# Performance work log

Measured on AMD Instinct MI355X. Metric: run time of the kernel, lower is better.

## Reference

```python
import jax, jax.numpy as jnp
import numpy as np

HEADS = 16
KV_HEADS = 4
DIM_HEAD = 64
DIM = 1024
B, N = 2, 2048


def setup_inputs() -> dict:
    key = jax.random.key(0)
    k1, k2, k3 = jax.random.split(key, 3)
    x = jax.random.normal(k1, (B, N, DIM), dtype=jnp.float32)
    Wq = jax.random.normal(k2, (DIM, HEADS * DIM_HEAD), dtype=jnp.float32) / np.sqrt(DIM)
    Wkv = jax.random.normal(k3, (DIM, 2 * KV_HEADS * DIM_HEAD), dtype=jnp.float32) / np.sqrt(DIM)
    k_scale = jnp.ones((HEADS, 1, DIM_HEAD), dtype=jnp.float32)
    return {"x": x, "Wq": Wq, "Wkv": Wkv, "k_scale": k_scale}


def reference(x, Wq, Wkv, k_scale):
    b, n, _ = x.shape
    g = HEADS // KV_HEADS  # query heads per kv head
    scale = DIM_HEAD ** -0.5
    # fused qkv projections (no bias)
    q = (x @ Wq).reshape(b, n, HEADS, DIM_HEAD)
    kv = x @ Wkv
    k, v = jnp.split(kv, 2, axis=-1)
    k = k.reshape(b, n, KV_HEADS, DIM_HEAD).transpose(0, 2, 1, 3)  # b k n d
    v = v.reshape(b, n, KV_HEADS, DIM_HEAD).transpose(0, 2, 1, 3)  # b k n d
    # group query heads: b, kv_heads, g, n, d
    qg = q.transpose(0, 2, 1, 3).reshape(b, KV_HEADS, g, n, DIM_HEAD)
    # per-query-head k scale, applied to the group-broadcast k (qk-norm)
    ks = k_scale.reshape(KV_HEADS, g, 1, DIM_HEAD)
    kk = k[:, :, None, :, :] * ks  # b k g n d
    dots = jnp.einsum('bkgid,bkgjd->bkgij', qg, kk) * scale
    attn = jax.nn.softmax(dots, axis=-1)
    out = jnp.einsum('bkgij,bkjd->bkgid', attn, v)  # v broadcast over g
    out = out.reshape(b, HEADS, n, DIM_HEAD).transpose(0, 2, 1, 3).reshape(b, n, HEADS * DIM_HEAD)
    return out
```

## Files before the change

### kernel.cpp

```cpp
#include <hip/hip_runtime.h>
#include <stdint.h>
#include <math.h>

typedef __attribute__((ext_vector_type(8))) __bf16 bf16x8;
typedef __attribute__((ext_vector_type(4))) float f32x4;
typedef __attribute__((ext_vector_type(16))) float f32x16;

__device__ __forceinline__ uint32_t f32_to_bf16_rne(float f) {
  union { float f; uint32_t u; } v; v.f = f;
  return (v.u + 0x7FFFu + ((v.u >> 16) & 1u)) >> 16;
}

__device__ __forceinline__ uint32_t cvt_pk_bf16(float lo, float hi) {
  uint32_t r;
  asm("v_cvt_pk_bf16_f32 %0, %1, %2" : "=v"(r) : "v"(lo), "v"(hi));
  return r;
}

__device__ __forceinline__ void gld16(void* lds, const void* g) {
  __builtin_amdgcn_global_load_lds(
      (__attribute__((address_space(1))) void*)(g),
      (__attribute__((address_space(3))) void*)(lds), 16, 0, 0);
}

__device__ __forceinline__ f32x4 mfma16(bf16x8 a, bf16x8 b, f32x4 c) {
  return __builtin_amdgcn_mfma_f32_16x16x32_bf16(a, b, c, 0, 0, 0);
}
__device__ __forceinline__ f32x16 mfma32(bf16x8 a, bf16x8 b, f32x16 c) {
  return __builtin_amdgcn_mfma_f32_32x32x16_bf16(a, b, c, 0, 0, 0);
}

#define LOG2E 1.44269504088896340736f

__global__ __launch_bounds__(256) void k_convert(const float* __restrict__ x,
                                                 const float* __restrict__ wq,
                                                 const float* __restrict__ wkv,
                                                 uint16_t* __restrict__ xb,
                                                 uint16_t* __restrict__ wt) {
  __shared__ float tile[64][65];
  int blk = blockIdx.x;
  int t = threadIdx.x;
  if (blk < 2048) {
    int i = blk * 256 + t;
    const float4* xv = (const float4*)x;
    float4 a = xv[2 * i], b2 = xv[2 * i + 1];
    uint32_t w0 = f32_to_bf16_rne(a.x) | (f32_to_bf16_rne(a.y) << 16);
    uint32_t w1 = f32_to_bf16_rne(a.z) | (f32_to_bf16_rne(a.w) << 16);
    uint32_t w2 = f32_to_bf16_rne(b2.x) | (f32_to_bf16_rne(b2.y) << 16);
    uint32_t w3 = f32_to_bf16_rne(b2.z) | (f32_to_bf16_rne(b2.w) << 16);
    ((uint4*)xb)[i] = make_uint4(w0, w1, w2, w3);
  } else {
    int blk2 = blk - 2048;
    int c0 = (blk2 % 24) * 64, k0 = (blk2 / 24) * 64;
    int col = t & 63, rq = t >> 6;
#pragma unroll
    for (int rr = 0; rr < 16; rr++) {
      int r = rr * 4 + rq;
      int c = c0 + col;
      float v = (c < 1024) ? wq[(uint64_t)(k0 + r) * 1024 + c]
                           : wkv[(uint64_t)(k0 + r) * 512 + (c - 1024)];
      tile[r][col] = v;
    }
    __syncthreads();
#pragma unroll
    for (int rr = 0; rr < 16; rr++) {
      int a = rr * 4 + rq;
      wt[(uint64_t)(c0 + a) * 1024 + k0 + col] = (uint16_t)f32_to_bf16_rne(tile[col][a]);
    }
  }
}

__global__ __launch_bounds__(256, 3) void k_proj_gemm(
    const uint16_t* __restrict__ xb, const uint16_t* __restrict__ wt,
    const float* __restrict__ kscale, uint16_t* __restrict__ q_ws,
    uint16_t* __restrict__ kf_ws, uint16_t* __restrict__ vf_ws) {
  __shared__ __align__(16) uint16_t ring[4][6144];
  int t = threadIdx.x;
  int w = t >> 6, l = t & 63;
  int lq = l & 15, lg = l >> 4;
  int m0 = blockIdx.x * 128, n0 = blockIdx.y * 64;
  int wr = w >> 1, wc = w & 1;
  f32x4 acc[4][2] = {};

  auto stage = [&](int slot, int k0) {
#pragma unroll
    for (int j = 0; j < 2; j++) {
      int tt = j * 256 + t;
      int r = tt >> 2, s = tt & 3;
      int sl = s ^ ((r >> 1) & 3);
      gld16((char*)&ring[slot][0] + (j * 256 + w * 64) * 16,
            xb + (uint64_t)(m0 + r) * 1024 + k0 + sl * 8);
    }
    {
      int r = t >> 2, s = t & 3;
      int sl = s ^ ((r >> 1) & 3);
      gld16((char*)&ring[slot][4096] + (w * 64) * 16,
            wt + (uint64_t)(n0 + r) * 1024 + k0 + sl * 8);
    }
  };

  struct PFrags { bf16x8 a[4]; bf16x8 b[2]; };
  auto readFrags = [&](PFrags& F, int slot) {
    const uint16_t* As = &ring[slot][0];
    const uint16_t* Bs = &ring[slot][4096];
#pragma unroll
    for (int m = 0; m < 4; m++) {
      int r = wr * 64 + m * 16 + lq;
      int s = lg ^ ((r >> 1) & 3);
      F.a[m] = *(const bf16x8*)(As + r * 32 + s * 8);
    }
#pragma unroll
    for (int n = 0; n < 2; n++) {
      int r = wc * 32 + n * 16 + lq;
      int s = lg ^ ((r >> 1) & 3);
      F.b[n] = *(const bf16x8*)(Bs + r * 32 + s * 8);
    }
  };

  auto pbody = [&](int tt2, PFrags& C, PFrags& N) {
    int kn = (tt2 + 3) * 32;
    if (kn > 992) kn = 992;
    stage((tt2 + 3) & 3, kn);
    __builtin_amdgcn_s_setprio(1);
#pragma unroll
    for (int m = 0; m < 4; m++)
#pragma unroll
      for (int n = 0; n < 2; n++)
        acc[m][n] = mfma16(C.a[m], C.b[n], acc[m][n]);
    __builtin_amdgcn_s_setprio(0);
    int tn = tt2 + 1;
    if (tn > 31) tn = 31;
    readFrags(N, tn & 3);
    asm volatile("s_waitcnt vmcnt(3) lgkmcnt(0)" ::: "memory");
    __builtin_amdgcn_s_barrier();
  };

  stage(0, 0);
  stage(1, 32);
  stage(2, 64);
  asm volatile("s_waitcnt vmcnt(3)" ::: "memory");
  __builtin_amdgcn_s_barrier();
  PFrags FA, FB;
  readFrags(FA, 0);
  for (int sp = 0; sp < 16; ++sp) {
    pbody(2 * sp, FA, FB);
    pbody(2 * sp + 1, FB, FA);
  }

#pragma unroll
  for (int m = 0; m < 4; m++)
#pragma unroll
    for (int n = 0; n < 2; n++)
#pragma unroll
      for (int jj = 0; jj < 4; jj++) {
        int row = m0 + wr * 64 + m * 16 + 4 * lg + jj;
        int col = n0 + wc * 32 + n * 16 + lq;
        float val = acc[m][n][jj];
        int b = row >> 11, nn = row & 2047;
        if (col < 1024) {
          val *= kscale[col] * 0.125f * LOG2E;
          q_ws[((uint64_t)((b * 16 + (col >> 6)) * 2048 + nn)) * 64 + (col & 63)] =
              (uint16_t)f32_to_bf16_rne(val);
        } else if (col < 1280) {
          int kvh = (col - 1024) >> 6;
          int d = col & 63;
          int gsu = nn >> 5, lrr = nn & 31;
          int mm = d >> 4, hh = (d >> 3) & 1, el = d & 7;
          kf_ws[(uint64_t)(b * 4 + kvh) * 131072 +
                (uint64_t)((((gsu * 4 + mm) * 64) + hh * 32 + lrr) * 8 + el)] =
              (uint16_t)f32_to_bf16_rne(val);
        } else {
          int kvh = (col - 1280) >> 6;
          int d = col & 63;
          int gsu = nn >> 5, jj2 = (nn >> 4) & 1, hh = (nn >> 3) & 1, el = nn & 7;
          int dd = d >> 5, lrr = d & 31;
          vf_ws[(uint64_t)(b * 4 + kvh) * 131072 +
                (uint64_t)((((gsu * 4 + dd * 2 + jj2) * 64) + hh * 32 + lrr) * 8 + el)] =
              (uint16_t)f32_to_bf16_rne(val);
        }
      }
}

__global__ __launch_bounds__(1024, 1) void k_attn(const uint16_t* __restrict__ q_ws,
                                                  const uint16_t* __restrict__ kf_ws,
                                                  const uint16_t* __restrict__ vf_ws,
                                                  float* __restrict__ out) {
  extern __shared__ __align__(16) char smem[];

  int t = threadIdx.x, w = t >> 6, l = t & 63;
  int lr = l & 31, hi = l >> 5;
  int wq = w & 7, half = w >> 3;
  int blk = blockIdx.x;
  int c = blk & 7, j = blk >> 3;
  int b = c >> 2, kvh = c & 3;
  int h = kvh * 4 + (j >> 3), qb = j & 7;

  const uint16_t* Qb = q_ws + (uint64_t)(b * 16 + h) * 2048 * 64;
  const uint16_t* Kb = kf_ws + (uint64_t)(b * 4 + kvh) * 131072;
  const uint16_t* Vb = vf_ws + (uint64_t)(b * 4 + kvh) * 131072;
  int qrow0 = qb * 256 + wq * 32;

  bf16x8 qfrag[4];
#pragma unroll
  for (int m = 0; m < 4; m++)
    qfrag[m] = *(const bf16x8*)(Qb + (uint64_t)(qrow0 + lr) * 64 + m * 16 + hi * 8);

  f32x16 oacc[2] = {};
  float l_run = 0.f;

  const uint16_t* SbW = (((w & 7) < 4) ? Kb : Vb) + (uint64_t)half * 65536 +
                        (uint64_t)(w & 3) * 512 + l * 8;
  char* dstW = smem + w * 1024 + l * 16;

  auto stage = [&](int slot, int sul) { gld16(dstW + slot * 16384, SbW + sul * 2048); };
  auto slotbase = [&](int slot) {
    return (const uint16_t*)(smem + slot * 16384 + half * 8192);
  };

  auto finish = [&](f32x16& Tc, const uint16_t* baseC) {
    float p[16];
#pragma unroll
    for (int e = 0; e < 16; e++) p[e] = __builtin_amdgcn_exp2f(Tc[e]);
    float sm0 = ((p[0] + p[1]) + (p[2] + p[3])) + ((p[4] + p[5]) + (p[6] + p[7]));
    float sm1 = ((p[8] + p[9]) + (p[10] + p[11])) + ((p[12] + p[13]) + (p[14] + p[15]));
    l_run += sm0 + sm1;

    bf16x8 pa[2];
#pragma unroll
    for (int jj = 0; jj < 2; jj++) {
      const float* pp = p + 8 * jj;
      uint32_t X = cvt_pk_bf16(pp[0], pp[1]);
      uint32_t Z = cvt_pk_bf16(pp[2], pp[3]);
      uint32_t Y = cvt_pk_bf16(pp[4], pp[5]);
      uint32_t W2 = cvt_pk_bf16(pp[6], pp[7]);
      asm volatile("v_permlane32_swap_b32 %0, %1" : "+v"(X), "+v"(Y));
      asm volatile("v_permlane32_swap_b32 %0, %1" : "+v"(Z), "+v"(W2));
      union { uint32_t u[4]; bf16x8 v; } pu;
      pu.u[0] = X; pu.u[1] = Z; pu.u[2] = Y; pu.u[3] = W2;
      pa[jj] = pu.v;
    }

    bf16x8 vf[4];
#pragma unroll
    for (int i = 0; i < 4; i++) vf[i] = *(const bf16x8*)(baseC + (4 + i) * 512 + l * 8);
    __builtin_amdgcn_s_setprio(1);
#pragma unroll
    for (int dd = 0; dd < 2; dd++)
#pragma unroll
      for (int jj = 0; jj < 2; jj++)
        oacc[dd] = mfma32(pa[jj], vf[dd * 2 + jj], oacc[dd]);
    __builtin_amdgcn_s_setprio(0);
  };

#pragma unroll
  for (int tt = 0; tt < 6; ++tt) stage(tt, tt);
  asm volatile("s_waitcnt vmcnt(4)" ::: "memory");
  __builtin_amdgcn_s_barrier();

  for (int iv = 0; iv < 16; ++iv) {
    int a = 2 * iv;
    int s0 = a + 6, s1 = a + 7;
    if (s0 > 31) s0 = 31;
    if (s1 > 31) s1 = 31;
    stage((a + 6) & 7, s0);
    stage((a + 7) & 7, s1);

    const uint16_t* baseA = slotbase(a & 7);
    const uint16_t* baseB = slotbase((a + 1) & 7);

    bf16x8 kfA[4], kfB[4];
#pragma unroll
    for (int m = 0; m < 4; m++) kfA[m] = *(const bf16x8*)(baseA + m * 512 + l * 8);
#pragma unroll
    for (int m = 0; m < 4; m++) kfB[m] = *(const bf16x8*)(baseB + m * 512 + l * 8);

    f32x16 Ta = {}, Tb = {};
    __builtin_amdgcn_s_setprio(1);
#pragma unroll
    for (int m = 0; m < 4; m++) Ta = mfma32(kfA[m], qfrag[m], Ta);
#pragma unroll
    for (int m = 0; m < 4; m++) Tb = mfma32(kfB[m], qfrag[m], Tb);
    __builtin_amdgcn_s_setprio(0);

    finish(Ta, baseA);
    finish(Tb, baseB);

    asm volatile("s_waitcnt vmcnt(4)" ::: "memory");
    __builtin_amdgcn_s_barrier();
  }

  l_run += __shfl_xor(l_run, 32);

  asm volatile("s_waitcnt vmcnt(0)" ::: "memory");
  __syncthreads();

  float* exch = (float*)smem;
  float* exl = (float*)(smem + 65536);
  if (half == 1) {
#pragma unroll
    for (int r = 0; r < 16; r++) {
      int qr = (r & 3) + 8 * (r >> 2) + 4 * hi;
      exch[wq * 2048 + qr * 64 + lr] = oacc[0][r];
      exch[wq * 2048 + qr * 64 + 32 + lr] = oacc[1][r];
    }
    if (hi == 0) exl[wq * 32 + lr] = l_run;
  }
  __syncthreads();
  if (half == 0) {
    l_run += exl[wq * 32 + lr];
    float inv = 1.0f / l_run;
#pragma unroll
    for (int r = 0; r < 16; r++) {
      int qr = (r & 3) + 8 * (r >> 2) + 4 * hi;
      float iv = __shfl(inv, qr);
      float o0 = oacc[0][r] + exch[wq * 2048 + qr * 64 + lr];
      float o1 = oacc[1][r] + exch[wq * 2048 + qr * 64 + 32 + lr];
      float* orow = out + (uint64_t)(b * 2048 + qrow0 + qr) * 1024 + h * 64 + lr;
      orow[0] = o0 * iv;
      orow[32] = o1 * iv;
    }
  }
}

extern "C" void kernel_launch(void* const* d_in, const int* in_sizes, int n_in,
                              void* d_out, int out_size, void* d_ws, size_t ws_size,
                              hipStream_t stream) {
  const float* x = (const float*)d_in[0];
  const float* wq = (const float*)d_in[1];
  const float* wkv = (const float*)d_in[2];
  const float* kscale = (const float*)d_in[3];
  float* out = (float*)d_out;
  char* ws = (char*)d_ws;
  uint16_t* xb = (uint16_t*)(ws);
  uint16_t* wt = (uint16_t*)(ws + (8ull << 20));
  uint16_t* q_ws = (uint16_t*)(ws + (11ull << 20));
  uint16_t* kf_ws = (uint16_t*)(ws + (19ull << 20));
  uint16_t* vf_ws = (uint16_t*)(ws + (21ull << 20));

  static bool attr_set = false;
  if (!attr_set) {
    (void)hipFuncSetAttribute((const void*)k_attn,
                              hipFuncAttributeMaxDynamicSharedMemorySize, 131072);
    attr_set = true;
  }

  k_convert<<<2432, 256, 0, stream>>>(x, wq, wkv, xb, wt);
  k_proj_gemm<<<dim3(32, 24), 256, 0, stream>>>(xb, wt, kscale, q_ws, kf_ws, vf_ws);
  k_attn<<<256, 1024, 131072, stream>>>(q_ws, kf_ws, vf_ws, out);
}
```

Before: 77.45 us.

## Halve attention block to 8 waves, each wave handling two query tiles

Each wave in the attention kernel now processes 64 query rows (two 32-row MFMA tiles) rather than 32, so the block shrinks from 16 to 8 waves. Every K and V fragment read from LDS is reused across both query tiles. The staging pipeline moves from 8 slots with two key blocks per iteration to 6 slots with one key block per iteration, and each thread issues two global-to-LDS loads per stage. This cuts LDS reads and block size, but doubles accumulator registers per wave and lowers the number of waves available to hide latency.

Measured after the change: 76.78 us. About the same (-0.9%).

```diff
diff --git a/kernel.cpp b/kernel.cpp
--- a/kernel.cpp
+++ b/kernel.cpp
@@ -181,15 +181,15 @@
       }
 }
 
-__global__ __launch_bounds__(1024, 1) void k_attn(const uint16_t* __restrict__ q_ws,
-                                                  const uint16_t* __restrict__ kf_ws,
-                                                  const uint16_t* __restrict__ vf_ws,
-                                                  float* __restrict__ out) {
+__global__ __launch_bounds__(512, 1) void k_attn(const uint16_t* __restrict__ q_ws,
+                                                 const uint16_t* __restrict__ kf_ws,
+                                                 const uint16_t* __restrict__ vf_ws,
+                                                 float* __restrict__ out) {
   extern __shared__ __align__(16) char smem[];
 
   int t = threadIdx.x, w = t >> 6, l = t & 63;
   int lr = l & 31, hi = l >> 5;
-  int wq = w & 7, half = w >> 3;
+  int qg = w & 3, half = w >> 2;
   int blk = blockIdx.x;
   int c = blk & 7, j = blk >> 3;
   int b = c >> 2, kvh = c & 3;
@@ -198,32 +198,39 @@
   const uint16_t* Qb = q_ws + (uint64_t)(b * 16 + h) * 2048 * 64;
   const uint16_t* Kb = kf_ws + (uint64_t)(b * 4 + kvh) * 131072;
   const uint16_t* Vb = vf_ws + (uint64_t)(b * 4 + kvh) * 131072;
-  int qrow0 = qb * 256 + wq * 32;
-
-  bf16x8 qfrag[4];
-#pragma unroll
-  for (int m = 0; m < 4; m++)
-    qfrag[m] = *(const bf16x8*)(Qb + (uint64_t)(qrow0 + lr) * 64 + m * 16 + hi * 8);
-
-  f32x16 oacc[2] = {};
-  float l_run = 0.f;
-
-  const uint16_t* SbW = (((w & 7) < 4) ? Kb : Vb) + (uint64_t)half * 65536 +
-                        (uint64_t)(w & 3) * 512 + l * 8;
-  char* dstW = smem + w * 1024 + l * 16;
-
-  auto stage = [&](int slot, int sul) { gld16(dstW + slot * 16384, SbW + sul * 2048); };
+  int qrow0 = qb * 256 + qg * 64;
+
+  bf16x8 qfA[4], qfB[4];
+#pragma unroll
+  for (int m = 0; m < 4; m++) {
+    qfA[m] = *(const bf16x8*)(Qb + (uint64_t)(qrow0 + lr) * 64 + m * 16 + hi * 8);
+    qfB[m] = *(const bf16x8*)(Qb + (uint64_t)(qrow0 + 32 + lr) * 64 + m * 16 + hi * 8);
+  }
+
+  f32x16 oaccA[2] = {}, oaccB[2] = {};
+  float lA = 0.f, lB = 0.f;
+
+  const uint16_t* SbW = ((qg < 2) ? Kb : Vb) + (uint64_t)half * 65536 +
+                        (uint64_t)((qg & 1) * 2) * 512 + l * 8;
+  char* dstW = smem + half * 8192 + ((qg < 2) ? 0 : 4096) + (qg & 1) * 2048 + l * 16;
+
+  auto stage = [&](int slot, int sul) {
+    char* d = dstW + slot * 16384;
+    const uint16_t* s = SbW + (uint64_t)sul * 2048;
+    gld16(d, s);
+    gld16(d + 1024, s + 512);
+  };
   auto slotbase = [&](int slot) {
     return (const uint16_t*)(smem + slot * 16384 + half * 8192);
   };
 
-  auto finish = [&](f32x16& Tc, const uint16_t* baseC) {
+  auto finish = [&](f32x16& Tc, const bf16x8* vf, f32x16* oacc, float& lsum) {
     float p[16];
 #pragma unroll
     for (int e = 0; e < 16; e++) p[e] = __builtin_amdgcn_exp2f(Tc[e]);
     float sm0 = ((p[0] + p[1]) + (p[2] + p[3])) + ((p[4] + p[5]) + (p[6] + p[7]));
     float sm1 = ((p[8] + p[9]) + (p[10] + p[11])) + ((p[12] + p[13]) + (p[14] + p[15]));
-    l_run += sm0 + sm1;
+    lsum += sm0 + sm1;
 
     bf16x8 pa[2];
 #pragma unroll
@@ -240,9 +247,6 @@
       pa[jj] = pu.v;
     }
 
-    bf16x8 vf[4];
-#pragma unroll
-    for (int i = 0; i < 4; i++) vf[i] = *(const bf16x8*)(baseC + (4 + i) * 512 + l * 8);
     __builtin_amdgcn_s_setprio(1);
 #pragma unroll
     for (int dd = 0; dd < 2; dd++)
@@ -253,43 +257,41 @@
   };
 
 #pragma unroll
-  for (int tt = 0; tt < 6; ++tt) stage(tt, tt);
-  asm volatile("s_waitcnt vmcnt(4)" ::: "memory");
+  for (int tt = 0; tt < 4; ++tt) stage(tt, tt);
+  asm volatile("s_waitcnt vmcnt(6)" ::: "memory");
   __builtin_amdgcn_s_barrier();
 
-  for (int iv = 0; iv < 16; ++iv) {
-    int a = 2 * iv;
-    int s0 = a + 6, s1 = a + 7;
-    if (s0 > 31) s0 = 31;
-    if (s1 > 31) s1 = 31;
-    stage((a + 6) & 7, s0);
-    stage((a + 7) & 7, s1);
-
-    const uint16_t* baseA = slotbase(a & 7);
-    const uint16_t* baseB = slotbase((a + 1) & 7);
-
-    bf16x8 kfA[4], kfB[4];
-#pragma unroll
-    for (int m = 0; m < 4; m++) kfA[m] = *(const bf16x8*)(baseA + m * 512 + l * 8);
-#pragma unroll
-    for (int m = 0; m < 4; m++) kfB[m] = *(const bf16x8*)(baseB + m * 512 + l * 8);
+  for (int su = 0; su < 32; ++su) {
+    int sn = su + 4;
+    if (sn > 31) sn = 31;
+    stage((su + 4) % 6, sn);
+
+    const uint16_t* base = slotbase(su % 6);
+    bf16x8 kf[4];
+#pragma unroll
+    for (int m = 0; m < 4; m++) kf[m] = *(const bf16x8*)(base + m * 512 + l * 8);
 
     f32x16 Ta = {}, Tb = {};
     __builtin_amdgcn_s_setprio(1);
 #pragma unroll
-    for (int m = 0; m < 4; m++) Ta = mfma32(kfA[m], qfrag[m], Ta);
-#pragma unroll
-    for (int m = 0; m < 4; m++) Tb = mfma32(kfB[m], qfrag[m], Tb);
+    for (int m = 0; m < 4; m++) Ta = mfma32(kf[m], qfA[m], Ta);
+#pragma unroll
+    for (int m = 0; m < 4; m++) Tb = mfma32(kf[m], qfB[m], Tb);
     __builtin_amdgcn_s_setprio(0);
 
-    finish(Ta, baseA);
-    finish(Tb, baseB);
-
-    asm volatile("s_waitcnt vmcnt(4)" ::: "memory");
+    bf16x8 vf[4];
+#pragma unroll
+    for (int i = 0; i < 4; i++) vf[i] = *(const bf16x8*)(base + (4 + i) * 512 + l * 8);
+
+    finish(Ta, vf, oaccA, lA);
+    finish(Tb, vf, oaccB, lB);
+
+    asm volatile("s_waitcnt vmcnt(6)" ::: "memory");
     __builtin_amdgcn_s_barrier();
   }
 
-  l_run += __shfl_xor(l_run, 32);
+  lA += __shfl_xor(lA, 32);
+  lB += __shfl_xor(lB, 32);
 
   asm volatile("s_waitcnt vmcnt(0)" ::: "memory");
   __syncthreads();
@@ -298,26 +300,40 @@
   float* exl = (float*)(smem + 65536);
   if (half == 1) {
 #pragma unroll
-    for (int r = 0; r < 16; r++) {
-      int qr = (r & 3) + 8 * (r >> 2) + 4 * hi;
-      exch[wq * 2048 + qr * 64 + lr] = oacc[0][r];
-      exch[wq * 2048 + qr * 64 + 32 + lr] = oacc[1][r];
-    }
-    if (hi == 0) exl[wq * 32 + lr] = l_run;
+    for (int sub = 0; sub < 2; sub++) {
+      f32x16* oacc = sub ? oaccB : oaccA;
+#pragma unroll
+      for (int r = 0; r < 16; r++) {
+        int qr = (r & 3) + 8 * (r >> 2) + 4 * hi;
+        exch[qg * 4096 + (sub * 32 + qr) * 64 + lr] = oacc[0][r];
+        exch[qg * 4096 + (sub * 32 + qr) * 64 + 32 + lr] = oacc[1][r];
+      }
+    }
+    if (hi == 0) {
+      exl[qg * 64 + lr] = lA;
+      exl[qg * 64 + 32 + lr] = lB;
+    }
   }
   __syncthreads();
   if (half == 0) {
-    l_run += exl[wq * 32 + lr];
-    float inv = 1.0f / l_run;
-#pragma unroll
-    for (int r = 0; r < 16; r++) {
-      int qr = (r & 3) + 8 * (r >> 2) + 4 * hi;
-      float iv = __shfl(inv, qr);
-      float o0 = oacc[0][r] + exch[wq * 2048 + qr * 64 + lr];
-      float o1 = oacc[1][r] + exch[wq * 2048 + qr * 64 + 32 + lr];
-      float* orow = out + (uint64_t)(b * 2048 + qrow0 + qr) * 1024 + h * 64 + lr;
-      orow[0] = o0 * iv;
-      orow[32] = o1 * iv;
+    lA += exl[qg * 64 + lr];
+    lB += exl[qg * 64 + 32 + lr];
+    float invA = 1.0f / lA, invB = 1.0f / lB;
+#pragma unroll
+    for (int sub = 0; sub < 2; sub++) {
+      f32x16* oacc = sub ? oaccB : oaccA;
+      float inv = sub ? invB : invA;
+#pragma unroll
+      for (int r = 0; r < 16; r++) {
+        int qr = (r & 3) + 8 * (r >> 2) + 4 * hi;
+        float iv = __shfl(inv, qr);
+        float o0 = oacc[0][r] + exch[qg * 4096 + (sub * 32 + qr) * 64 + lr];
+        float o1 = oacc[1][r] + exch[qg * 4096 + (sub * 32 + qr) * 64 + 32 + lr];
+        float* orow =
+            out + (uint64_t)(b * 2048 + qrow0 + sub * 32 + qr) * 1024 + h * 64 + lr;
+        orow[0] = o0 * iv;
+        orow[32] = o1 * iv;
+      }
     }
   }
 }
@@ -340,11 +356,11 @@
   static bool attr_set = false;
   if (!attr_set) {
     (void)hipFuncSetAttribute((const void*)k_attn,
-                              hipFuncAttributeMaxDynamicSharedMemorySize, 131072);
+                              hipFuncAttributeMaxDynamicSharedMemorySize, 98304);
     attr_set = true;
   }
 
   k_convert<<<2432, 256, 0, stream>>>(x, wq, wkv, xb, wt);
   k_proj_gemm<<<dim3(32, 24), 256, 0, stream>>>(xb, wt, kscale, q_ws, kf_ws, vf_ws);
-  k_attn<<<256, 1024, 131072, stream>>>(q_ws, kf_ws, vf_ws, out);
-}
+  k_attn<<<256, 512, 98304, stream>>>(q_ws, kf_ws, vf_ws, out);
+}
```
